# Optimization experiments

Hardware: AMD Instinct MI355X
Metric: run time of the kernel (lower is better)

## Reference

```python
import jax, jax.numpy as jnp
import numpy as np

D, DK, DV, H = 1024, 64, 1024, 16
DVH = DV // H  # per-head value dim
EPS = 1e-5


def _layer_norm(x, g, b):
    mu = jnp.mean(x, axis=-1, keepdims=True)
    var = jnp.var(x, axis=-1, keepdims=True)
    return (x - mu) * jax.lax.rsqrt(var + EPS) * g + b


def setup_inputs() -> dict:
    key = jax.random.key(0)
    ks = jax.random.split(key, 12)
    s = lambda k, shape, fan_in: jax.random.normal(k, shape, jnp.float32) / np.sqrt(fan_in)
    return {
        "x": jax.random.normal(ks[0], (2, 2048, D), jnp.float32),
        "Wq": s(ks[1], (H, D, DK), D),
        "Wk": s(ks[2], (H, D, DK), D),
        "Wv": s(ks[3], (H, D, DVH), D),
        "Wo": s(ks[4], (DV, D), DV),
        "ln1_g": jnp.ones((D,), jnp.float32),
        "ln1_b": jnp.zeros((D,), jnp.float32),
        "W1": s(ks[5], (D, 4 * D), D),
        "b1": jnp.zeros((4 * D,), jnp.float32),
        "W2": s(ks[6], (4 * D, D), 4 * D),
        "b2": jnp.zeros((D,), jnp.float32),
        "ln2_g": jnp.ones((D,), jnp.float32),
        "ln2_b": jnp.zeros((D,), jnp.float32),
    }


def reference(x, Wq, Wk, Wv, Wo, ln1_g, ln1_b, W1, b1, W2, b2, ln2_g, ln2_b):
    B, S, _ = x.shape
    # per-head projections (vectorized over the head loop of the original)
    q = jnp.einsum("bsd,hdk->bhsk", x, Wq)
    k = jnp.einsum("bsd,hdk->bhsk", x, Wk)
    v = jnp.einsum("bsd,hdv->bhsv", x, Wv)
    scores = jnp.einsum("bhsk,bhtk->bhst", q, k) / np.sqrt(DK).astype(np.float32)
    attn = jax.nn.softmax(scores, axis=-1)
    o = jnp.einsum("bhst,bhtv->bhsv", attn, v)  # [B,H,S,DVH]
    o = o.transpose(0, 2, 1, 3).reshape(B, S, DV)  # concat heads
    attn_out = o @ Wo
    x1 = _layer_norm(attn_out + x, ln1_g, ln1_b)
    ffn = jax.nn.relu(x1 @ W1 + b1) @ W2 + b2
    return _layer_norm(ffn + x1, ln2_g, ln2_b)
```

## Files before the change

### kernel.cpp

```cpp
#include <hip/hip_runtime.h>
#include <hip/hip_bf16.h>

typedef unsigned short u16;
typedef unsigned int u32;
typedef short short8 __attribute__((ext_vector_type(8)));
typedef float fx4 __attribute__((ext_vector_type(4)));
typedef u32 ux4 __attribute__((ext_vector_type(4)));
typedef u32 ux2 __attribute__((ext_vector_type(2)));

__device__ __forceinline__ float b2f(u16 x) {
  return __uint_as_float(((u32)x) << 16);
}
__device__ __forceinline__ u16 f2b(float f) {
  u32 u = __float_as_uint(f);
  u += 0x7fffu + ((u >> 16) & 1u);
  return (u16)(u >> 16);
}
__device__ __forceinline__ u32 cvtpk(float a, float b) {
  u32 r;
  asm("v_cvt_pk_bf16_f32 %0, %1, %2" : "=v"(r) : "v"(a), "v"(b));
  return r;
}

__device__ __forceinline__ void load16(const u16* g, u16* l) {
  __builtin_amdgcn_global_load_lds(
      (__attribute__((address_space(1))) void*)(u16*)g,
      (__attribute__((address_space(3))) void*)l, 16, 0, 0);
}

__global__ __launch_bounds__(256) void cvt_f2b_kernel(
    const float* __restrict__ in, u16* __restrict__ out)
{
  int i = (blockIdx.x * 256 + threadIdx.x) * 4;
  fx4 v = *(const fx4*)(in + i);
  u16 o4[4];
#pragma unroll
  for (int j = 0; j < 4; ++j) o4[j] = f2b(v[j]);
  *(uint2*)(out + i) = *(uint2*)o4;
}

__global__ __launch_bounds__(256) void transpose_f2b_kernel(
    const float* __restrict__ in, u16* __restrict__ out,
    int R, int C, int out_ld)
{
  __shared__ __align__(16) u16 tile[32][33];
  int tx = threadIdx.x, ty = threadIdx.y;
  int c0 = blockIdx.x * 32, r0 = blockIdx.y * 32;
  const float* inb = in + (size_t)blockIdx.z * R * C;
  u16* outb = out + (size_t)blockIdx.z * C * out_ld;
#pragma unroll
  for (int i = 0; i < 4; ++i)
    tile[ty + i * 8][tx] = f2b(inb[(size_t)(r0 + ty + i * 8) * C + c0 + tx]);
  __syncthreads();
#pragma unroll
  for (int i = 0; i < 4; ++i)
    outb[(size_t)(c0 + ty + i * 8) * out_ld + r0 + tx] = tile[tx][ty + i * 8];
}

__global__ __launch_bounds__(256) void transpose_b2b_kernel(
    const u16* __restrict__ in, u16* __restrict__ out, int in_ld, int out_ld)
{
  __shared__ __align__(16) u16 tile[32][33];
  int tx = threadIdx.x, ty = threadIdx.y;
  int c0 = blockIdx.x * 32, r0 = blockIdx.y * 32;
#pragma unroll
  for (int i = 0; i < 4; ++i)
    tile[ty + i * 8][tx] = in[(size_t)(r0 + ty + i * 8) * in_ld + c0 + tx];
  __syncthreads();
#pragma unroll
  for (int i = 0; i < 4; ++i)
    out[(size_t)(c0 + ty + i * 8) * out_ld + r0 + tx] = tile[tx][ty + i * 8];
}

__global__ __launch_bounds__(256, 2) void gemm_bt(
    const u16* __restrict__ A, const u16* __restrict__ BT,
    const float* __restrict__ bias, void* __restrict__ Cp,
    int M, int N, int K, int flags)
{
  __shared__ __align__(16) u16 As[2][4096];
  __shared__ __align__(16) u16 Bs[2][4096];
  int tid = threadIdx.x;
  int lane = tid & 63, wid = tid >> 6;
  int l15 = lane & 15, quad = lane >> 4;
  int wm = wid >> 1, wn = wid & 1;
  int m0 = blockIdx.y * 128, n0 = blockIdx.x * 128;

  int srow = wid * 16 + (lane >> 2);
  int sswz = (((lane >> 2) & 3) + ((lane >> 4) & 3)) & 3;
  int gch = (lane & 3) ^ sswz;
  const u16* gA = A + (size_t)(m0 + srow) * K + gch * 8;
  const u16* gB = BT + (size_t)(n0 + srow) * K + gch * 8;
  size_t gstep = (size_t)64 * K;
  u16* lA = &As[0][wid * 512];
  u16* lB = &Bs[0][wid * 512];

  int rswz = ((l15 & 3) + (l15 >> 2)) & 3;
  int rphys = ((quad ^ rswz) & 3) << 3;

  fx4 acc[4][4];
#pragma unroll
  for (int i = 0; i < 4; ++i)
#pragma unroll
    for (int j = 0; j < 4; ++j) acc[i][j] = fx4{0.f, 0.f, 0.f, 0.f};

  int nt = K >> 5;
  load16(gA,         lA);
  load16(gA + gstep, lA + 2048);
  load16(gB,         lB);
  load16(gB + gstep, lB + 2048);

  for (int kt = 0; kt < nt; ++kt) {
    __syncthreads();
    if (kt + 1 < nt) {
      int buf = (kt + 1) & 1;
      const u16* ga = gA + (kt + 1) * 32;
      const u16* gb = gB + (kt + 1) * 32;
      load16(ga,         lA + buf * 4096);
      load16(ga + gstep, lA + buf * 4096 + 2048);
      load16(gb,         lB + buf * 4096);
      load16(gb + gstep, lB + buf * 4096 + 2048);
    }
    const u16* Ab = As[kt & 1];
    const u16* Bb = Bs[kt & 1];
    short8 af[4], bf[4];
#pragma unroll
    for (int t = 0; t < 4; ++t)
      af[t] = *(const short8*)&Ab[(wm * 64 + t * 16 + l15) * 32 + rphys];
#pragma unroll
    for (int t = 0; t < 4; ++t)
      bf[t] = *(const short8*)&Bb[(wn * 64 + t * 16 + l15) * 32 + rphys];
#pragma unroll
    for (int tm = 0; tm < 4; ++tm)
#pragma unroll
      for (int tn = 0; tn < 4; ++tn)
        acc[tm][tn] = __builtin_amdgcn_mfma_f32_16x16x32_bf16(
            af[tm], bf[tn], acc[tm][tn], 0, 0, 0);
  }

  bool obf = flags & 1, hb = flags & 2, rl = flags & 4;
#pragma unroll
  for (int tn = 0; tn < 4; ++tn) {
    int col = n0 + wn * 64 + tn * 16 + l15;
    float bv = hb ? bias[col] : 0.0f;
#pragma unroll
    for (int tm = 0; tm < 4; ++tm) {
      int row = m0 + wm * 64 + tm * 16 + (quad << 2);
#pragma unroll
      for (int r = 0; r < 4; ++r) {
        float v = acc[tm][tn][r] + bv;
        if (rl) v = fmaxf(v, 0.0f);
        size_t idx = (size_t)(row + r) * N + col;
        if (obf) ((u16*)Cp)[idx] = f2b(v);
        else ((float*)Cp)[idx] = v;
      }
    }
  }
}

__global__ __launch_bounds__(256, 2) void gemm_bt_n64(
    const u16* __restrict__ A, const u16* __restrict__ BT,
    const float* __restrict__ bias, void* __restrict__ Cp,
    int M, int N, int K, int flags)
{
  __shared__ __align__(16) u16 As[2][4096];
  __shared__ __align__(16) u16 Bs[2][2048];
  int tid = threadIdx.x;
  int lane = tid & 63, wid = tid >> 6;
  int l15 = lane & 15, quad = lane >> 4;
  int wm = wid >> 1, wn = wid & 1;

  int nx = gridDim.x, ny = gridDim.y;
  int total = nx * ny * (int)gridDim.z;
  int cpx = total >> 3;
  int lin = blockIdx.x + nx * (blockIdx.y + ny * blockIdx.z);
  int swb = (lin & 7) * cpx + (lin >> 3);
  int bx = swb % nx;
  int t2 = swb / nx;
  int by = t2 % ny;
  int bz = t2 / ny;

  int m0 = by * 128, n0 = bx * 64;
  int zz = bz;
  int kc = K / (int)gridDim.z;

  int srow = wid * 16 + (lane >> 2);
  int sswz = (((lane >> 2) & 3) + ((lane >> 4) & 3)) & 3;
  int gch = (lane & 3) ^ sswz;
  const u16* gA = A + (size_t)(m0 + srow) * K + zz * kc + gch * 8;
  const u16* gB = BT + (size_t)(n0 + srow) * K + zz * kc + gch * 8;
  size_t gstep = (size_t)64 * K;
  u16* lA = &As[0][wid * 512];
  u16* lB = &Bs[0][wid * 512];

  int rswz = ((l15 & 3) + (l15 >> 2)) & 3;
  int rphys = ((quad ^ rswz) & 3) << 3;

  fx4 acc[4][2];
#pragma unroll
  for (int i = 0; i < 4; ++i)
#pragma unroll
    for (int j = 0; j < 2; ++j) acc[i][j] = fx4{0.f, 0.f, 0.f, 0.f};

  int nt = kc >> 5;
  load16(gA,         lA);
  load16(gA + gstep, lA + 2048);
  load16(gB,         lB);

  for (int kt = 0; kt < nt; ++kt) {
    __syncthreads();
    if (kt + 1 < nt) {
      int buf = (kt + 1) & 1;
      const u16* ga = gA + (kt + 1) * 32;
      const u16* gb = gB + (kt + 1) * 32;
      load16(ga,         lA + buf * 4096);
      load16(ga + gstep, lA + buf * 4096 + 2048);
      load16(gb,         lB + buf * 2048);
    }
    const u16* Ab = As[kt & 1];
    const u16* Bb = Bs[kt & 1];
    short8 af[4], bf[2];
#pragma unroll
    for (int t = 0; t < 4; ++t)
      af[t] = *(const short8*)&Ab[(wm * 64 + t * 16 + l15) * 32 + rphys];
#pragma unroll
    for (int t = 0; t < 2; ++t)
      bf[t] = *(const short8*)&Bb[(wn * 32 + t * 16 + l15) * 32 + rphys];
#pragma unroll
    for (int tm = 0; tm < 4; ++tm)
#pragma unroll
      for (int tn = 0; tn < 2; ++tn)
        acc[tm][tn] = __builtin_amdgcn_mfma_f32_16x16x32_bf16(
            af[tm], bf[tn], acc[tm][tn], 0, 0, 0);
  }

  bool obf = flags & 1, hb = flags & 2, rl = flags & 4;
  u16* cb16 = (u16*)Cp + (size_t)zz * M * N;
  float* cf32 = (float*)Cp + (size_t)zz * M * N;
#pragma unroll
  for (int tn = 0; tn < 2; ++tn) {
    int col = n0 + wn * 32 + tn * 16 + l15;
    float bv = hb ? bias[col] : 0.0f;
#pragma unroll
    for (int tm = 0; tm < 4; ++tm) {
      int row = m0 + wm * 64 + tm * 16 + (quad << 2);
#pragma unroll
      for (int r = 0; r < 4; ++r) {
        float v = acc[tm][tn][r] + bv;
        if (rl) v = fmaxf(v, 0.0f);
        size_t idx = (size_t)(row + r) * N + col;
        if (obf) cb16[idx] = f2b(v);
        else cf32[idx] = v;
      }
    }
  }
}

__global__ __launch_bounds__(256, 2) void attn_kernel(
    const u16* __restrict__ qkv, const u16* __restrict__ vT,
    u16* __restrict__ o)
{
  __shared__ __align__(16) u16 Ks[2][4096];
  __shared__ __align__(16) u16 Vs[2][4096];
  int tid = threadIdx.x;
  int lane = tid & 63, wid = tid >> 6;
  int l15 = lane & 15, quad = lane >> 4;
  int b = blockIdx.z, h = blockIdx.y;
  int q0 = blockIdx.x * 128 + wid * 32;

  const u16* qbA = qkv + (size_t)(b * 2048 + q0 + l15) * 3072 + h * 64 + (quad << 3);
  short8 qA0 = *(const short8*)qbA;
  short8 qA1 = *(const short8*)(qbA + 32);
  const u16* qbB = qbA + (size_t)16 * 3072;
  short8 qB0 = *(const short8*)qbB;
  short8 qB1 = *(const short8*)(qbB + 32);

  int srow = tid >> 3;
  int gc8 = ((tid & 7) ^ (srow & 7)) << 3;
  const u16* kg = qkv + (size_t)(b * 2048 + srow) * 3072 + 1024 + h * 64 + gc8;
  const u16* vg = vT + (size_t)(h * 64 + srow) * 4096 + b * 2048 + gc8;
  u16* lk = &Ks[0][wid * 512];
  u16* lv = &Vs[0][wid * 512];

  int lq = l15 >> 2;
  int rs = ((((lq & 1) << 1) | (lq >> 1)) << 2) | (l15 & 3);
  int sk = rs & 7;

  fx4 oaccA[4], oaccB[4];
  float sumA = 0.0f, sumB = 0.0f;
#pragma unroll
  for (int i = 0; i < 4; ++i) {
    oaccA[i] = fx4{0.f, 0.f, 0.f, 0.f};
    oaccB[i] = fx4{0.f, 0.f, 0.f, 0.f};
  }

  load16(kg,             lk);
  load16(kg + 32 * 3072, lk + 2048);
  load16(vg,             lv);
  load16(vg + 32 * 4096, lv + 2048);

  int swz = l15 & 7;
  const float SC = 0.18033688011112042f;
  for (int kt = 0; kt < 32; ++kt) {
    __syncthreads();
    if (kt + 1 < 32) {
      int buf = (kt + 1) & 1;
      const u16* kgn = kg + (size_t)(kt + 1) * 64 * 3072;
      const u16* vgn = vg + (kt + 1) * 64;
      load16(kgn,             lk + buf * 4096);
      load16(kgn + 32 * 3072, lk + buf * 4096 + 2048);
      load16(vgn,             lv + buf * 4096);
      load16(vgn + 32 * 4096, lv + buf * 4096 + 2048);
    }
    const u16* Kb = Ks[kt & 1];
    const u16* Vb = Vs[kt & 1];

    fx4 scA[4], scB[4];
    __builtin_amdgcn_s_setprio(1);
#pragma unroll
    for (int sub = 0; sub < 4; ++sub) {
      const u16* rp = &Kb[(sub * 16 + rs) * 64];
      short8 kf0 = *(const short8*)&rp[((quad ^ sk) & 7) << 3];
      short8 kf1 = *(const short8*)&rp[(((4 | quad) ^ sk) & 7) << 3];
      scA[sub] = fx4{0.f, 0.f, 0.f, 0.f};
      scA[sub] = __builtin_amdgcn_mfma_f32_16x16x32_bf16(kf0, qA0, scA[sub], 0, 0, 0);
      scA[sub] = __builtin_amdgcn_mfma_f32_16x16x32_bf16(kf1, qA1, scA[sub], 0, 0, 0);
      scB[sub] = fx4{0.f, 0.f, 0.f, 0.f};
      scB[sub] = __builtin_amdgcn_mfma_f32_16x16x32_bf16(kf0, qB0, scB[sub], 0, 0, 0);
      scB[sub] = __builtin_amdgcn_mfma_f32_16x16x32_bf16(kf1, qB1, scB[sub], 0, 0, 0);
    }
    __builtin_amdgcn_s_setprio(0);

    u32 WA[4][2], WB[4][2];
    float psA = 0.0f, psB = 0.0f;
#pragma unroll
    for (int sub = 0; sub < 4; ++sub) {
      float a0 = __builtin_amdgcn_exp2f(scA[sub][0] * SC);
      float a1 = __builtin_amdgcn_exp2f(scA[sub][1] * SC);
      float a2 = __builtin_amdgcn_exp2f(scA[sub][2] * SC);
      float a3 = __builtin_amdgcn_exp2f(scA[sub][3] * SC);
      psA += (a0 + a1) + (a2 + a3);
      WA[sub][0] = cvtpk(a0, a1);
      WA[sub][1] = cvtpk(a2, a3);
      float b0 = __builtin_amdgcn_exp2f(scB[sub][0] * SC);
      float b1 = __builtin_amdgcn_exp2f(scB[sub][1] * SC);
      float b2 = __builtin_amdgcn_exp2f(scB[sub][2] * SC);
      float b3 = __builtin_amdgcn_exp2f(scB[sub][3] * SC);
      psB += (b0 + b1) + (b2 + b3);
      WB[sub][0] = cvtpk(b0, b1);
      WB[sub][1] = cvtpk(b2, b3);
    }
    sumA += psA;
    sumB += psB;

    ux2 eA00 = __builtin_amdgcn_permlane32_swap(WA[0][0], WA[1][0], false, false);
    ux2 eA01 = __builtin_amdgcn_permlane32_swap(WA[0][1], WA[1][1], false, false);
    ux2 eA10 = __builtin_amdgcn_permlane32_swap(WA[2][0], WA[3][0], false, false);
    ux2 eA11 = __builtin_amdgcn_permlane32_swap(WA[2][1], WA[3][1], false, false);
    short8 pa1A = __builtin_bit_cast(short8, ux4{eA00[0], eA01[0], eA00[1], eA01[1]});
    short8 pa2A = __builtin_bit_cast(short8, ux4{eA10[0], eA11[0], eA10[1], eA11[1]});
    ux2 eB00 = __builtin_amdgcn_permlane32_swap(WB[0][0], WB[1][0], false, false);
    ux2 eB01 = __builtin_amdgcn_permlane32_swap(WB[0][1], WB[1][1], false, false);
    ux2 eB10 = __builtin_amdgcn_permlane32_swap(WB[2][0], WB[3][0], false, false);
    ux2 eB11 = __builtin_amdgcn_permlane32_swap(WB[2][1], WB[3][1], false, false);
    short8 pa1B = __builtin_bit_cast(short8, ux4{eB00[0], eB01[0], eB00[1], eB01[1]});
    short8 pa2B = __builtin_bit_cast(short8, ux4{eB10[0], eB11[0], eB10[1], eB11[1]});

    __builtin_amdgcn_s_setprio(1);
#pragma unroll
    for (int dt = 0; dt < 4; ++dt) {
      const u16* rp = &Vb[(dt * 16 + l15) * 64];
      short8 vf0 = *(const short8*)&rp[((quad ^ swz) & 7) << 3];
      short8 vf1 = *(const short8*)&rp[(((4 | quad) ^ swz) & 7) << 3];
      oaccA[dt] = __builtin_amdgcn_mfma_f32_16x16x32_bf16(pa1A, vf0, oaccA[dt], 0, 0, 0);
      oaccA[dt] = __builtin_amdgcn_mfma_f32_16x16x32_bf16(pa2A, vf1, oaccA[dt], 0, 0, 0);
      oaccB[dt] = __builtin_amdgcn_mfma_f32_16x16x32_bf16(pa1B, vf0, oaccB[dt], 0, 0, 0);
      oaccB[dt] = __builtin_amdgcn_mfma_f32_16x16x32_bf16(pa2B, vf1, oaccB[dt], 0, 0, 0);
    }
    __builtin_amdgcn_s_setprio(0);
  }
  sumA += __shfl_xor(sumA, 16, 64);
  sumA += __shfl_xor(sumA, 32, 64);
  sumB += __shfl_xor(sumB, 16, 64);
  sumB += __shfl_xor(sumB, 32, 64);
  fx4 invA, invB;
#pragma unroll
  for (int r = 0; r < 4; ++r) {
    invA[r] = 1.0f / __shfl(sumA, (quad << 2) + r, 64);
    invB[r] = 1.0f / __shfl(sumB, (quad << 2) + r, 64);
  }
#pragma unroll
  for (int dt = 0; dt < 4; ++dt) {
    int col = h * 64 + dt * 16 + l15;
#pragma unroll
    for (int r = 0; r < 4; ++r) {
      size_t rowA = (size_t)(b * 2048 + q0 + (quad << 2) + r);
      o[rowA * 1024 + col] = f2b(oaccA[dt][r] * invA[r]);
      o[(rowA + 16) * 1024 + col] = f2b(oaccB[dt][r] * invB[r]);
    }
  }
}

__global__ __launch_bounds__(256) void ln_kernel(
    const float* __restrict__ main0, const float* __restrict__ main1,
    const float* __restrict__ res, const float* __restrict__ cbias,
    const float* __restrict__ g, const float* __restrict__ beta,
    u16* __restrict__ out_b, float* __restrict__ out_f)
{
  __shared__ float red[8];
  int row = blockIdx.x, tid = threadIdx.x;
  size_t base = (size_t)row * 1024 + tid * 4;
  fx4 v = *(const fx4*)(main0 + base);
  fx4 v1 = *(const fx4*)(main1 + base);
  fx4 rv = *(const fx4*)(res + base);
#pragma unroll
  for (int i = 0; i < 4; ++i) v[i] += v1[i] + rv[i];
  if (cbias) {
    fx4 cb = *(const fx4*)(cbias + tid * 4);
#pragma unroll
    for (int i = 0; i < 4; ++i) v[i] += cb[i];
  }
  float s = v[0] + v[1] + v[2] + v[3];
  float sq = v[0] * v[0] + v[1] * v[1] + v[2] * v[2] + v[3] * v[3];
#pragma unroll
  for (int off = 32; off >= 1; off >>= 1) {
    s += __shfl_xor(s, off, 64);
    sq += __shfl_xor(sq, off, 64);
  }
  int wid = tid >> 6, lane = tid & 63;
  if (lane == 0) { red[wid] = s; red[wid + 4] = sq; }
  __syncthreads();
  float S = red[0] + red[1] + red[2] + red[3];
  float SQ = red[4] + red[5] + red[6] + red[7];
  float mean = S * (1.0f / 1024.0f);
  float var = SQ * (1.0f / 1024.0f) - mean * mean;
  float rs = rsqrtf(var + 1e-5f);
  fx4 gv = *(const fx4*)(g + tid * 4);
  fx4 bv = *(const fx4*)(beta + tid * 4);
  float of[4];
#pragma unroll
  for (int i = 0; i < 4; ++i) of[i] = (v[i] - mean) * rs * gv[i] + bv[i];
  if (out_f) *(fx4*)(out_f + base) = *(const fx4*)of;
  if (out_b) {
    u16 o4[4];
#pragma unroll
    for (int i = 0; i < 4; ++i) o4[i] = f2b(of[i]);
    *(uint2*)(out_b + base) = *(uint2*)o4;
  }
}

extern "C" void kernel_launch(void* const* d_in, const int* in_sizes, int n_in,
                              void* d_out, int out_size, void* d_ws, size_t ws_size,
                              hipStream_t stream) {
  (void)in_sizes; (void)n_in; (void)out_size; (void)ws_size;
  const float* x     = (const float*)d_in[0];
  const float* Wq    = (const float*)d_in[1];
  const float* Wk    = (const float*)d_in[2];
  const float* Wv    = (const float*)d_in[3];
  const float* Wo    = (const float*)d_in[4];
  const float* g1    = (const float*)d_in[5];
  const float* bb1   = (const float*)d_in[6];
  const float* W1    = (const float*)d_in[7];
  const float* bias1 = (const float*)d_in[8];
  const float* W2    = (const float*)d_in[9];
  const float* bias2 = (const float*)d_in[10];
  const float* g2    = (const float*)d_in[11];
  const float* bb2   = (const float*)d_in[12];

  char* ws = (char*)d_ws;
  const size_t MB = 1048576;
  u16* xb     = (u16*)(ws);
  u16* wqkvT  = (u16*)(ws + 8 * MB);
  u16* woT    = (u16*)(ws + 38 * MB);
  u16* qkv    = (u16*)(ws + 40 * MB);
  u16* vT     = (u16*)(ws + 64 * MB);
  u16* ob     = (u16*)(ws + 72 * MB);
  float* aout = (float*)(ws);
  u16* x1     = (u16*)(ws + 64 * MB);
  float* x1f  = (float*)(ws + 40 * MB);
  u16* w1T    = (u16*)(ws + 56 * MB);
  u16* w2T    = (u16*)(ws);
  u16* hbuf   = (u16*)(ws + 8 * MB);
  float* ffn  = (float*)(ws + 56 * MB);

  dim3 tb(32, 8, 1);
  cvt_f2b_kernel<<<4096, 256, 0, stream>>>(x, xb);
  transpose_f2b_kernel<<<dim3(2, 32, 16), tb, 0, stream>>>(Wq, wqkvT,           1024, 64, 1024);
  transpose_f2b_kernel<<<dim3(2, 32, 16), tb, 0, stream>>>(Wk, wqkvT + 1048576, 1024, 64, 1024);
  transpose_f2b_kernel<<<dim3(2, 32, 16), tb, 0, stream>>>(Wv, wqkvT + 2097152, 1024, 64, 1024);
  transpose_f2b_kernel<<<dim3(32, 32, 1), tb, 0, stream>>>(Wo, woT, 1024, 1024, 1024);

  gemm_bt<<<dim3(24, 32), 256, 0, stream>>>(xb, wqkvT, nullptr, qkv, 4096, 3072, 1024, 1);
  transpose_b2b_kernel<<<dim3(32, 128), tb, 0, stream>>>(qkv + 2048, vT, 3072, 4096);
  attn_kernel<<<dim3(16, 16, 2), 256, 0, stream>>>(qkv, vT, ob);
  gemm_bt_n64<<<dim3(16, 32, 2), 256, 0, stream>>>(ob, woT, nullptr, aout, 4096, 1024, 1024, 0);
  ln_kernel<<<4096, 256, 0, stream>>>(aout, aout + 4194304, x, nullptr, g1, bb1, x1, x1f);
  transpose_f2b_kernel<<<dim3(128, 32, 1), tb, 0, stream>>>(W1, w1T, 1024, 4096, 1024);
  transpose_f2b_kernel<<<dim3(32, 128, 1), tb, 0, stream>>>(W2, w2T, 4096, 1024, 4096);
  gemm_bt<<<dim3(32, 32), 256, 0, stream>>>(x1, w1T, bias1, hbuf, 4096, 4096, 1024, 1 | 2 | 4);
  gemm_bt_n64<<<dim3(16, 32, 2), 256, 0, stream>>>(hbuf, w2T, nullptr, ffn, 4096, 1024, 4096, 0);
  ln_kernel<<<4096, 256, 0, stream>>>(ffn, ffn + 4194304, x1f, bias2, g2, bb2, nullptr, (float*)d_out);
}
```

Measured before the change: 368.8 us.

## Widen split-K GEMM to 128x128 tiles with 64-deep K steps

Replaces the 128x64-tile, K=32-step split-K GEMM used for the output projection and the second FFN matmul with a 128x128-tile kernel that stages 64-wide K slices and uses an 8-way XOR swizzle in LDS. Each warp now computes a 64x64 sub-tile, which raises MFMA work per LDS read and halves the number of barriers per K. The cost is four times the shared memory (64KB per block) and twice the accumulator registers, which may reduce occupancy. It also halves the grid to 512 blocks.

```diff
diff --git a/kernel.cpp b/kernel.cpp
--- a/kernel.cpp
+++ b/kernel.cpp
@@ -157,88 +157,93 @@
   }
 }
 
-__global__ __launch_bounds__(256, 2) void gemm_bt_n64(
+__global__ __launch_bounds__(256, 2) void gemm_bt_k64(
     const u16* __restrict__ A, const u16* __restrict__ BT,
     const float* __restrict__ bias, void* __restrict__ Cp,
     int M, int N, int K, int flags)
 {
-  __shared__ __align__(16) u16 As[2][4096];
-  __shared__ __align__(16) u16 Bs[2][2048];
+  __shared__ __align__(16) u16 As[2][8192];
+  __shared__ __align__(16) u16 Bs[2][8192];
   int tid = threadIdx.x;
   int lane = tid & 63, wid = tid >> 6;
   int l15 = lane & 15, quad = lane >> 4;
   int wm = wid >> 1, wn = wid & 1;
 
-  int nx = gridDim.x, ny = gridDim.y;
-  int total = nx * ny * (int)gridDim.z;
-  int cpx = total >> 3;
-  int lin = blockIdx.x + nx * (blockIdx.y + ny * blockIdx.z);
-  int swb = (lin & 7) * cpx + (lin >> 3);
-  int bx = swb % nx;
-  int t2 = swb / nx;
-  int by = t2 % ny;
-  int bz = t2 / ny;
-
-  int m0 = by * 128, n0 = bx * 64;
-  int zz = bz;
+  int bx = blockIdx.x, by = blockIdx.y, bz = blockIdx.z;
+  if (gridDim.z > 1) {
+    int nx = gridDim.x, ny = gridDim.y;
+    int total = nx * ny * (int)gridDim.z;
+    int cpx = total >> 3;
+    int lin = bx + nx * (by + ny * bz);
+    int swb = (lin & 7) * cpx + (lin >> 3);
+    bx = swb % nx;
+    int t2 = swb / nx;
+    by = t2 % ny;
+    bz = t2 / ny;
+  }
+  int m0 = by * 128, n0 = bx * 128;
   int kc = K / (int)gridDim.z;
 
-  int srow = wid * 16 + (lane >> 2);
-  int sswz = (((lane >> 2) & 3) + ((lane >> 4) & 3)) & 3;
-  int gch = (lane & 3) ^ sswz;
-  const u16* gA = A + (size_t)(m0 + srow) * K + zz * kc + gch * 8;
-  const u16* gB = BT + (size_t)(n0 + srow) * K + zz * kc + gch * 8;
-  size_t gstep = (size_t)64 * K;
+  int r8 = lane >> 3;
+  int clog = (lane & 7) ^ r8;
+  const u16* gA = A + (size_t)(m0 + wid * 8 + r8) * K + bz * kc + clog * 8;
+  const u16* gB = BT + (size_t)(n0 + wid * 8 + r8) * K + bz * kc + clog * 8;
+  size_t gstep = (size_t)32 * K;
   u16* lA = &As[0][wid * 512];
   u16* lB = &Bs[0][wid * 512];
 
-  int rswz = ((l15 & 3) + (l15 >> 2)) & 3;
-  int rphys = ((quad ^ rswz) & 3) << 3;
-
-  fx4 acc[4][2];
+  fx4 acc[4][4];
 #pragma unroll
   for (int i = 0; i < 4; ++i)
 #pragma unroll
-    for (int j = 0; j < 2; ++j) acc[i][j] = fx4{0.f, 0.f, 0.f, 0.f};
-
-  int nt = kc >> 5;
-  load16(gA,         lA);
-  load16(gA + gstep, lA + 2048);
-  load16(gB,         lB);
+    for (int j = 0; j < 4; ++j) acc[i][j] = fx4{0.f, 0.f, 0.f, 0.f};
+
+  int nt = kc >> 6;
+#pragma unroll
+  for (int i = 0; i < 4; ++i) {
+    load16(gA + i * gstep, lA + i * 2048);
+    load16(gB + i * gstep, lB + i * 2048);
+  }
 
   for (int kt = 0; kt < nt; ++kt) {
     __syncthreads();
     if (kt + 1 < nt) {
       int buf = (kt + 1) & 1;
-      const u16* ga = gA + (kt + 1) * 32;
-      const u16* gb = gB + (kt + 1) * 32;
-      load16(ga,         lA + buf * 4096);
-      load16(ga + gstep, lA + buf * 4096 + 2048);
-      load16(gb,         lB + buf * 2048);
+      const u16* ga = gA + (kt + 1) * 64;
+      const u16* gb = gB + (kt + 1) * 64;
+#pragma unroll
+      for (int i = 0; i < 4; ++i) {
+        load16(ga + i * gstep, lA + buf * 8192 + i * 2048);
+        load16(gb + i * gstep, lB + buf * 8192 + i * 2048);
+      }
     }
     const u16* Ab = As[kt & 1];
     const u16* Bb = Bs[kt & 1];
-    short8 af[4], bf[2];
-#pragma unroll
-    for (int t = 0; t < 4; ++t)
-      af[t] = *(const short8*)&Ab[(wm * 64 + t * 16 + l15) * 32 + rphys];
-#pragma unroll
-    for (int t = 0; t < 2; ++t)
-      bf[t] = *(const short8*)&Bb[(wn * 32 + t * 16 + l15) * 32 + rphys];
-#pragma unroll
-    for (int tm = 0; tm < 4; ++tm)
-#pragma unroll
-      for (int tn = 0; tn < 2; ++tn)
-        acc[tm][tn] = __builtin_amdgcn_mfma_f32_16x16x32_bf16(
-            af[tm], bf[tn], acc[tm][tn], 0, 0, 0);
+#pragma unroll
+    for (int s = 0; s < 2; ++s) {
+      int ch = (((s << 2) | quad) ^ (l15 & 7)) << 3;
+      short8 af[4], bf[4];
+#pragma unroll
+      for (int t = 0; t < 4; ++t)
+        af[t] = *(const short8*)&Ab[(wm * 64 + t * 16 + l15) * 64 + ch];
+#pragma unroll
+      for (int t = 0; t < 4; ++t)
+        bf[t] = *(const short8*)&Bb[(wn * 64 + t * 16 + l15) * 64 + ch];
+#pragma unroll
+      for (int tm = 0; tm < 4; ++tm)
+#pragma unroll
+        for (int tn = 0; tn < 4; ++tn)
+          acc[tm][tn] = __builtin_amdgcn_mfma_f32_16x16x32_bf16(
+              af[tm], bf[tn], acc[tm][tn], 0, 0, 0);
+    }
   }
 
   bool obf = flags & 1, hb = flags & 2, rl = flags & 4;
-  u16* cb16 = (u16*)Cp + (size_t)zz * M * N;
-  float* cf32 = (float*)Cp + (size_t)zz * M * N;
-#pragma unroll
-  for (int tn = 0; tn < 2; ++tn) {
-    int col = n0 + wn * 32 + tn * 16 + l15;
+  u16* cb16 = (u16*)Cp + (size_t)bz * M * N;
+  float* cf32 = (float*)Cp + (size_t)bz * M * N;
+#pragma unroll
+  for (int tn = 0; tn < 4; ++tn) {
+    int col = n0 + wn * 64 + tn * 16 + l15;
     float bv = hb ? bias[col] : 0.0f;
 #pragma unroll
     for (int tm = 0; tm < 4; ++tm) {
@@ -492,11 +497,11 @@
   gemm_bt<<<dim3(24, 32), 256, 0, stream>>>(xb, wqkvT, nullptr, qkv, 4096, 3072, 1024, 1);
   transpose_b2b_kernel<<<dim3(32, 128), tb, 0, stream>>>(qkv + 2048, vT, 3072, 4096);
   attn_kernel<<<dim3(16, 16, 2), 256, 0, stream>>>(qkv, vT, ob);
-  gemm_bt_n64<<<dim3(16, 32, 2), 256, 0, stream>>>(ob, woT, nullptr, aout, 4096, 1024, 1024, 0);
+  gemm_bt_k64<<<dim3(8, 32, 2), 256, 0, stream>>>(ob, woT, nullptr, aout, 4096, 1024, 1024, 0);
   ln_kernel<<<4096, 256, 0, stream>>>(aout, aout + 4194304, x, nullptr, g1, bb1, x1, x1f);
   transpose_f2b_kernel<<<dim3(128, 32, 1), tb, 0, stream>>>(W1, w1T, 1024, 4096, 1024);
   transpose_f2b_kernel<<<dim3(32, 128, 1), tb, 0, stream>>>(W2, w2T, 4096, 1024, 4096);
   gemm_bt<<<dim3(32, 32), 256, 0, stream>>>(x1, w1T, bias1, hbuf, 4096, 4096, 1024, 1 | 2 | 4);
-  gemm_bt_n64<<<dim3(16, 32, 2), 256, 0, stream>>>(hbuf, w2T, nullptr, ffn, 4096, 1024, 4096, 0);
+  gemm_bt_k64<<<dim3(8, 32, 2), 256, 0, stream>>>(hbuf, w2T, nullptr, ffn, 4096, 1024, 4096, 0);
   ln_kernel<<<4096, 256, 0, stream>>>(ffn, ffn + 4194304, x1f, bias2, g2, bb2, nullptr, (float*)d_out);
 }
```

After: 352.1 us. -4.5%, faster.
